# Kernel tuning notes

Hardware: AMD Instinct MI355X
Metric: run time of the kernel (lower is better)

## Reference

```python
import jax, jax.numpy as jnp
import numpy as np

TEMPERATURE = 0.5


def setup_inputs() -> dict:
    key = jax.random.key(0)
    k1, k2 = jax.random.split(key)
    N, D = 4096, 128
    z_i = jax.random.normal(k1, (N, D), dtype=jnp.float32)
    z_j = jax.random.normal(k2, (N, D), dtype=jnp.float32)
    return {"z_i": z_i, "z_j": z_j}


def reference(z_i, z_j):
    # make_permutation interleaves the two views: rows are
    # [z_i[0], z_j[0], z_i[1], z_j[1], ...]  -> shape [2N, D]
    N, D = z_i.shape
    z = jnp.stack([z_i, z_j], axis=1).reshape(2 * N, D)
    # cosine similarity: zTz / (||z_a|| * ||z_b||) == normalized rows matmul
    norm = jnp.linalg.norm(z, axis=-1, keepdims=True)  # [2N, 1]
    s = (z @ z.T) / (norm @ norm.T)                    # [2N, 2N]
    e = jnp.exp(s / TEMPERATURE)
    idx = jnp.arange(2 * N)
    partner = idx ^ 1                                   # (2k <-> 2k+1) positive pairs
    numerator = e[idx, partner]                         # [2N]
    denominator = jnp.sum(e, axis=-1) - jnp.diagonal(e)  # row-sum minus self-sim
    # original sums all 2N per-sample losses then divides by 2N == mean
    return jnp.mean(-jnp.log(numerator / denominator))
```

## Files before the change

kernel.cpp:

```cpp
#include <hip/hip_runtime.h>
#include <hip/hip_bf16.h>

#define N_PAIR 4096
#define N_ROW  8192
#define DIM    128
#define NX     8

typedef __attribute__((ext_vector_type(4))) float f32x4;

__device__ inline float fast_exp2(float x) {
#if __has_builtin(__builtin_amdgcn_exp2f)
    return __builtin_amdgcn_exp2f(x);
#else
    float r; asm("v_exp_f32 %0, %1" : "=v"(r) : "v"(x)); return r;
#endif
}
__device__ inline float fast_log2(float x) {
#if __has_builtin(__builtin_amdgcn_logf)
    return __builtin_amdgcn_logf(x);
#else
    float r; asm("v_log_f32 %0, %1" : "=v"(r) : "v"(x)); return r;
#endif
}

__global__ __launch_bounds__(256) void k_prep(const float* __restrict__ zi,
                                              const float* __restrict__ zj,
                                              unsigned char* __restrict__ zh8,
                                              float* __restrict__ pd,
                                              float* __restrict__ rowsum) {
    const int wid  = threadIdx.x >> 6;
    const int lane = threadIdx.x & 63;
    const int k    = blockIdx.x * 4 + wid;
    float2 a = *(const float2*)&zi[k * DIM + lane * 2];
    float2 b = *(const float2*)&zj[k * DIM + lane * 2];
    float ssi = a.x * a.x + a.y * a.y;
    float ssj = b.x * b.x + b.y * b.y;
    float dot = a.x * b.x + a.y * b.y;
#pragma unroll
    for (int off = 1; off < 64; off <<= 1) {
        ssi += __shfl_xor(ssi, off);
        ssj += __shfl_xor(ssj, off);
        dot += __shfl_xor(dot, off);
    }
    const float invi = rsqrtf(ssi), invj = rsqrtf(ssj);
    unsigned int pi = __builtin_amdgcn_cvt_pk_fp8_f32(a.x * invi, a.y * invi, 0, false);
    unsigned int pj = __builtin_amdgcn_cvt_pk_fp8_f32(b.x * invj, b.y * invj, 0, false);
    ((unsigned short*)zh8)[(2 * k)     * (DIM / 2) + lane] = (unsigned short)pi;
    ((unsigned short*)zh8)[(2 * k + 1) * (DIM / 2) + lane] = (unsigned short)pj;
    if (lane == 0) {
        pd[k] = dot * invi * invj;
        rowsum[2 * k]     = 0.f;
        rowsum[2 * k + 1] = 0.f;
    }
}

__global__ __launch_bounds__(512, 4) void k_simsum(const unsigned char* __restrict__ zh8,
                                                   float* __restrict__ rowsum) {
    __shared__ unsigned char Bs[8 * 8192];
    const int tid  = threadIdx.x;
    const int lane = tid & 63;
    const int wid  = tid >> 6;
    const int wr   = wid >> 2, wc = wid & 3;
    const int l15  = lane & 15, lhi = lane >> 4;
    const int by   = blockIdx.y;
    const int bx0  = blockIdx.x * NX;
    const int row0 = by * 128 + wr * 64;
    const int wbase = wid * 8192;

    long a[4][4];
#pragma unroll
    for (int kk = 0; kk < 4; ++kk)
#pragma unroll
        for (int m = 0; m < 4; ++m)
            a[kk][m] = *(const long*)&zh8[(row0 + m * 16 + l15) * DIM + kk * 32 + lhi * 8];

    auto stage = [&](int ct, int buf) {
#pragma unroll
        for (int i = 0; i < 4; ++i) {
            const int rl = i * 8 + (lane >> 3);
            const int g  = (lane & 7) ^ (rl & 7);
            const unsigned char* src = zh8 + (ct * 128 + wc * 32 + rl) * DIM + g * 16;
            __builtin_amdgcn_global_load_lds(
                (const __attribute__((address_space(1))) void*)src,
                (__attribute__((address_space(3))) void*)(&Bs[wbase + buf * 4096 + i * 1024]),
                16, 0, 0);
        }
    };

    const float K2E = 2.8853900817779268f;
    float rs[4] = {0.f, 0.f, 0.f, 0.f};

    stage(bx0, 0);
    asm volatile("s_waitcnt vmcnt(0)" ::: "memory");

    int cur = 0;
#pragma unroll 1
    for (int t = 0; t < NX; ++t) {
        if (t + 1 < NX) stage(bx0 + t + 1, cur ^ 1);
        const int bx = bx0 + t;
        f32x4 accT[2][4] = {};
#pragma unroll
        for (int kk = 0; kk < 4; ++kk) {
            long b[2];
#pragma unroll
            for (int n = 0; n < 2; ++n) {
                const int rowb = n * 16 + l15;
                const int byteoff = wbase + cur * 4096 + rowb * 128 +
                    (((kk * 2 + (lhi >> 1)) ^ (l15 & 7)) << 4) + ((lhi & 1) << 3);
                b[n] = *(const long*)&Bs[byteoff];
            }
            __builtin_amdgcn_s_setprio(1);
#pragma unroll
            for (int n = 0; n < 2; ++n)
#pragma unroll
                for (int m = 0; m < 4; ++m)
                    accT[n][m] = __builtin_amdgcn_mfma_f32_16x16x32_fp8_fp8(b[n], a[kk][m], accT[n][m], 0, 0, 0);
            __builtin_amdgcn_s_setprio(0);
        }
        if (bx == by) {
#pragma unroll
            for (int m = 0; m < 4; ++m) {
                const int rloc = wr * 64 + m * 16 + l15;
                float s0 = 0.f, s1 = 0.f;
#pragma unroll
                for (int n = 0; n < 2; ++n)
#pragma unroll
                    for (int r = 0; r < 4; ++r) {
                        const int cloc = wc * 32 + n * 16 + lhi * 4 + r;
                        float v = fast_exp2(K2E * accT[n][m][r]);
                        v = (cloc == rloc) ? 0.f : v;
                        if (n == 0) s0 += v; else s1 += v;
                    }
                rs[m] += s0 + s1;
            }
        } else {
#pragma unroll
            for (int m = 0; m < 4; ++m) {
                float s0 = 0.f, s1 = 0.f;
#pragma unroll
                for (int n = 0; n < 2; ++n)
#pragma unroll
                    for (int r = 0; r < 4; ++r) {
                        float v = fast_exp2(K2E * accT[n][m][r]);
                        if (n == 0) s0 += v; else s1 += v;
                    }
                rs[m] += s0 + s1;
            }
        }
        if (t + 1 < NX) {
            asm volatile("s_waitcnt vmcnt(0)" ::: "memory");
            cur ^= 1;
        }
    }

#pragma unroll
    for (int m = 0; m < 4; ++m) {
        rs[m] += __shfl_xor(rs[m], 16);
        rs[m] += __shfl_xor(rs[m], 32);
    }
    if (lane < 16) {
#pragma unroll
        for (int m = 0; m < 4; ++m)
            atomicAdd(&rowsum[row0 + m * 16 + lane], rs[m]);
    }
}

__global__ __launch_bounds__(1024) void k_loss(const float* __restrict__ rowsum,
                                               const float* __restrict__ pd,
                                               float* __restrict__ out) {
    const int tid  = threadIdx.x;
    const int lane = tid & 63;
    const int wid  = tid >> 6;
    const float LN2 = 0.6931471805599453f;
    float local = 0.f;
    for (int i = tid; i < N_ROW; i += 1024)
        local += fast_log2(rowsum[i]) * LN2 - 2.f * pd[i >> 1];
#pragma unroll
    for (int off = 1; off < 64; off <<= 1) local += __shfl_xor(local, off);
    __shared__ float wsum[16];
    if (lane == 0) wsum[wid] = local;
    __syncthreads();
    if (tid == 0) {
        float s = 0.f;
#pragma unroll
        for (int w = 0; w < 16; ++w) s += wsum[w];
        out[0] = s * (1.f / (float)N_ROW);
    }
}

extern "C" void kernel_launch(void* const* d_in, const int* in_sizes, int n_in,
                              void* d_out, int out_size, void* d_ws, size_t ws_size,
                              hipStream_t stream) {
    const float* zi = (const float*)d_in[0];
    const float* zj = (const float*)d_in[1];
    char* ws = (char*)d_ws;
    unsigned char* zh8 = (unsigned char*)ws;
    float* rowsum = (float*)(ws + 2 * 1024 * 1024);
    float* pd     = (float*)(ws + 2 * 1024 * 1024 + 32 * 1024);

    k_prep<<<N_PAIR / 4, 256, 0, stream>>>(zi, zj, zh8, pd, rowsum);
    dim3 grid(64 / NX, 64);
    k_simsum<<<grid, 512, 0, stream>>>(zh8, rowsum);
    k_loss<<<1, 1024, 0, stream>>>(rowsum, pd, (float*)d_out);
}
```

Baseline: 34.19 us.

## Use scaled 16x16x128 FP8 MFMA and reduce row sums in LDS before global atomics

Replaces the four K=32 FP8 MFMAs per tile with a single gfx950 mfma_scale 16x16x128 f8f6f4 instruction using unit scales. Operands are loaded as 32-byte vectors from global and from the swizzled LDS layout. The aim is to cut MFMA issue count and LDS read instructions. It also accumulates per-wave row sums with LDS atomics, so each block issues only 128 global atomics instead of one set per wave. The risk is that the operand lane/K ordering for the scaled instruction may not match the new loads; a mismatch would give wrong dot products.

```diff
diff --git a/kernel.cpp b/kernel.cpp
--- a/kernel.cpp
+++ b/kernel.cpp
@@ -7,6 +7,8 @@
 #define NX     8
 
 typedef __attribute__((ext_vector_type(4))) float f32x4;
+typedef __attribute__((ext_vector_type(4))) int   i32x4;
+typedef __attribute__((ext_vector_type(8))) int   i32x8;
 
 __device__ inline float fast_exp2(float x) {
 #if __has_builtin(__builtin_amdgcn_exp2f)
@@ -57,6 +59,7 @@
 __global__ __launch_bounds__(512, 4) void k_simsum(const unsigned char* __restrict__ zh8,
                                                    float* __restrict__ rowsum) {
     __shared__ unsigned char Bs[8 * 8192];
+    __shared__ float rsum_lds[128];
     const int tid  = threadIdx.x;
     const int lane = tid & 63;
     const int wid  = tid >> 6;
@@ -67,12 +70,18 @@
     const int row0 = by * 128 + wr * 64;
     const int wbase = wid * 8192;
 
-    long a[4][4];
-#pragma unroll
-    for (int kk = 0; kk < 4; ++kk)
-#pragma unroll
-        for (int m = 0; m < 4; ++m)
-            a[kk][m] = *(const long*)&zh8[(row0 + m * 16 + l15) * DIM + kk * 32 + lhi * 8];
+    if (tid < 128) rsum_lds[tid] = 0.f;
+    __syncthreads();
+
+    i32x8 a[4];
+#pragma unroll
+    for (int m = 0; m < 4; ++m) {
+        const unsigned char* ap = &zh8[(row0 + m * 16 + l15) * DIM + lhi * 32];
+        union { i32x4 h[2]; i32x8 v; } u;
+        u.h[0] = *(const i32x4*)ap;
+        u.h[1] = *(const i32x4*)(ap + 16);
+        a[m] = u.v;
+    }
 
     auto stage = [&](int ct, int buf) {
 #pragma unroll
@@ -88,6 +97,7 @@
     };
 
     const float K2E = 2.8853900817779268f;
+    const int   SC1 = 0x7F7F7F7F;
     float rs[4] = {0.f, 0.f, 0.f, 0.f};
 
     stage(bx0, 0);
@@ -98,25 +108,27 @@
     for (int t = 0; t < NX; ++t) {
         if (t + 1 < NX) stage(bx0 + t + 1, cur ^ 1);
         const int bx = bx0 + t;
-        f32x4 accT[2][4] = {};
-#pragma unroll
-        for (int kk = 0; kk < 4; ++kk) {
-            long b[2];
-#pragma unroll
-            for (int n = 0; n < 2; ++n) {
-                const int rowb = n * 16 + l15;
-                const int byteoff = wbase + cur * 4096 + rowb * 128 +
-                    (((kk * 2 + (lhi >> 1)) ^ (l15 & 7)) << 4) + ((lhi & 1) << 3);
-                b[n] = *(const long*)&Bs[byteoff];
-            }
-            __builtin_amdgcn_s_setprio(1);
-#pragma unroll
-            for (int n = 0; n < 2; ++n)
-#pragma unroll
-                for (int m = 0; m < 4; ++m)
-                    accT[n][m] = __builtin_amdgcn_mfma_f32_16x16x32_fp8_fp8(b[n], a[kk][m], accT[n][m], 0, 0, 0);
-            __builtin_amdgcn_s_setprio(0);
-        }
+        i32x8 b[2];
+#pragma unroll
+        for (int n = 0; n < 2; ++n) {
+            const int rowb = n * 16 + l15;
+            const int base = wbase + cur * 4096 + rowb * 128;
+            union { i32x4 h[2]; i32x8 v; } u;
+            u.h[0] = *(const i32x4*)&Bs[base + (((lhi * 2 + 0) ^ (l15 & 7)) << 4)];
+            u.h[1] = *(const i32x4*)&Bs[base + (((lhi * 2 + 1) ^ (l15 & 7)) << 4)];
+            b[n] = u.v;
+        }
+        f32x4 accT[2][4];
+        __builtin_amdgcn_s_setprio(1);
+#pragma unroll
+        for (int n = 0; n < 2; ++n)
+#pragma unroll
+            for (int m = 0; m < 4; ++m)
+                accT[n][m] = __builtin_amdgcn_mfma_scale_f32_16x16x128_f8f6f4(
+                    b[n], a[m], (f32x4){0.f, 0.f, 0.f, 0.f},
+                    0, 0,
+                    0, SC1, 0, SC1);
+        __builtin_amdgcn_s_setprio(0);
         if (bx == by) {
 #pragma unroll
             for (int m = 0; m < 4; ++m) {
@@ -161,8 +173,10 @@
     if (lane < 16) {
 #pragma unroll
         for (int m = 0; m < 4; ++m)
-            atomicAdd(&rowsum[row0 + m * 16 + lane], rs[m]);
-    }
+            atomicAdd(&rsum_lds[wr * 64 + m * 16 + lane], rs[m]);
+    }
+    __syncthreads();
+    if (tid < 128) atomicAdd(&rowsum[by * 128 + tid], rsum_lds[tid]);
 }
 
 __global__ __launch_bounds__(1024) void k_loss(const float* __restrict__ rowsum,
```

After: 31.68 us. -7.4%, faster.
